# Performance work log

Hardware: AMD Instinct MI355X
Metric: run time of the kernel (lower is better)

The kernel has to match this reference:

```python
import jax, jax.numpy as jnp
import numpy as np

# ----- static layer configuration (mirrors __init__ / _precompute_cg_tensor) -----
NODE_LS = [0, 0, 1, 1]          # node_l_values (multiplicity expressed via repetition; node_multiplicity=1)
EDGE_SH = 1                      # edge_sh_degree
H_LS = NODE_LS + NODE_LS + [0]   # l-values of h = [f_src, f_tgt, d]
H_DIMS = [2 * l + 1 for l in H_LS]
H_OFF = np.concatenate([[0], np.cumsum(H_DIMS)])
A_DIMS = [2 * l + 1 for l in range(EDGE_SH + 1)]
A_OFF = np.concatenate([[0], np.cumsum(A_DIMS)])
O_DIMS = [2 * l + 1 for l in NODE_LS]
O_OFF = np.concatenate([[0], np.cumsum(O_DIMS)])
F_DIM = int(O_OFF[-1])           # 8
A_DIM = int(A_OFF[-1])           # 4
N_NODES, N_EDGES = 100000, 1600000
MLP_DIMS = [2 * len(NODE_LS) + 1, 64, 32, len(NODE_LS)]  # 9 -> 64 -> 32 -> 4

def _levi_civita():
    e = np.zeros((3, 3, 3), np.float32)
    e[0, 1, 2] = e[1, 2, 0] = e[2, 0, 1] = 1.0
    e[0, 2, 1] = e[2, 1, 0] = e[1, 0, 2] = -1.0
    return e

# real SO(3) Clebsch-Gordan tensors (e3nn wigner_3j normalization: full contraction norm 1)
_CG = {
    (0, 0, 0): np.ones((1, 1, 1), np.float32),
    (0, 1, 1): (np.eye(3, dtype=np.float32) / np.sqrt(3.0)).reshape(1, 3, 3),
    (1, 0, 1): (np.eye(3, dtype=np.float32) / np.sqrt(3.0)).reshape(3, 1, 3),
    (1, 1, 0): (np.eye(3, dtype=np.float32) / np.sqrt(3.0)).reshape(3, 3, 1),
    (1, 1, 1): _levi_civita() / np.sqrt(6.0),
}

CONNECTIONS = []  # (h_idx, a_l, out_idx, cg[h,a,o]) -- same enumeration order as the torch loop
for _h_idx, _hl in enumerate(H_LS):
    for _al in range(EDGE_SH + 1):
        for _oi, _ol in enumerate(NODE_LS):
            if abs(_hl - _al) <= _ol <= _hl + _al and (_hl, _al, _ol) in _CG:
                CONNECTIONS.append((_h_idx, _al, _oi, jnp.asarray(_CG[(_hl, _al, _ol)])))


def _invariants(x):
    # s_i = [f_{l=0}, ||f_{l=1}||, ...] per l-slot (multiplicity 1)
    outs = []
    for i, l in enumerate(NODE_LS):
        s, e = int(O_OFF[i]), int(O_OFF[i + 1])
        if l == 0:
            outs.append(x[:, s:e])
        else:
            outs.append(jnp.linalg.norm(x[:, s:e], axis=1, keepdims=True))
    return jnp.concatenate(outs, axis=1)


def setup_inputs() -> dict:
    ks = jax.random.split(jax.random.key(0), 10)
    edge_index = jax.random.randint(ks[0], (2, N_EDGES), 0, N_NODES)
    f = jax.random.normal(ks[1], (N_NODES, F_DIM), jnp.float32)
    d = jax.random.uniform(ks[2], (N_EDGES, 1), jnp.float32)
    a = jax.random.normal(ks[3], (N_EDGES, A_DIM), jnp.float32)
    w1 = jax.random.normal(ks[4], (EDGE_SH + 1,), jnp.float32) * 0.1
    w2 = jax.random.normal(ks[5], (EDGE_SH + 1,), jnp.float32) * 0.1
    W0 = jax.random.normal(ks[6], (MLP_DIMS[0], MLP_DIMS[1]), jnp.float32) / np.sqrt(MLP_DIMS[0])
    b0 = jnp.zeros((MLP_DIMS[1],), jnp.float32)
    W1 = jax.random.normal(ks[7], (MLP_DIMS[1], MLP_DIMS[2]), jnp.float32) / np.sqrt(MLP_DIMS[1])
    b1 = jnp.zeros((MLP_DIMS[2],), jnp.float32)
    W2 = jax.random.normal(ks[8], (MLP_DIMS[2], MLP_DIMS[3]), jnp.float32) / np.sqrt(MLP_DIMS[2])
    b2 = jnp.zeros((MLP_DIMS[3],), jnp.float32)
    return {"edge_index": edge_index, "f": f, "d": d, "a": a, "w1": w1, "w2": w2,
            "W0": W0, "b0": b0, "W1": W1, "b1": b1, "W2": W2, "b2": b2}


def reference(edge_index, f, d, a, w1, w2, W0, b0, W1, b1, W2, b2):
    src, tgt = edge_index[0], edge_index[1]
    n = f.shape[0]
    h = jnp.concatenate([f[src], f[tgt], d], axis=1)  # [E, 17]
    messages = jnp.zeros((h.shape[0], F_DIM), f.dtype)
    for h_idx, a_l, out_idx, cg in CONNECTIONS:
        hs, he = int(H_OFF[h_idx]), int(H_OFF[h_idx + 1])
        as_, ae = int(A_OFF[a_l]), int(A_OFF[a_l + 1])
        os_, oe = int(O_OFF[out_idx]), int(O_OFF[out_idx + 1])
        raw = jnp.einsum('hao,eh,ea->eo', cg, h[:, hs:he], a[:, as_:ae])  # [E, 2*out_l+1]
        msg = jnp.tanh(w2[a_l] * jnp.tanh(w1[a_l] * raw))
        messages = messages.at[:, os_:oe].add(msg)
    agg = jax.ops.segment_sum(messages, tgt, num_segments=n)          # [N, 8]
    dist_sum = jax.ops.segment_sum(d, tgt, num_segments=n)           # [N, 1]
    counts = jax.ops.segment_sum(jnp.ones((h.shape[0],), f.dtype), tgt, num_segments=n)
    avg_d = dist_sum / (counts[:, None] + 1e-8)
    psi_in = jnp.concatenate([_invariants(f), _invariants(agg), avg_d], axis=1)  # [N, 9]
    x = jax.nn.relu(psi_in @ W0 + b0)
    x = jax.nn.relu(x @ W1 + b1)
    gates = jax.nn.sigmoid(x @ W2 + b2)  # [N, 4]
    gate_full = jnp.concatenate(
        [jnp.repeat(gates[:, i:i + 1], O_DIMS[i], axis=1) for i in range(len(NODE_LS))], axis=1)
    return f + gate_full * agg
```

## Files before the change

### kernel.cpp

```cpp
#include <hip/hip_runtime.h>
#include <math.h>

#define IS3 0.57735026918962576f
#define IS6 0.40824829046386302f

#define SHIFT 11
#define BSZ   2048
#define CAP   36864u
#define SEG   10
#define MQ    4096.0f
#define IMQ   (1.0f/4096.0f)

__device__ __forceinline__ float fastrcp(float x) { return __builtin_amdgcn_rcpf(x); }

__device__ __forceinline__ float Tnl(float x, float tw1, float w2) {
    float e = __expf(tw1 * x);
    float u = 1.0f - 2.0f * fastrcp(e + 1.0f);
    float z = w2 * u;
    float z2 = z * z;
    float p = __builtin_fmaf(z2, 0.133333333f, -0.333333333f);
    return __builtin_fmaf(z * z2, p, z);
}

__device__ __forceinline__ int q16(float x) {
    int v = (int)rintf(x * MQ);
    v = v >  32767 ?  32767 : v;
    v = v < -32768 ? -32768 : v;
    return v;
}

__global__ __launch_bounds__(1024) void route_kernel(
    const int* __restrict__ ei, const float* __restrict__ f,
    const float* __restrict__ d, const float* __restrict__ a,
    const float* __restrict__ w1p, const float* __restrict__ w2p,
    unsigned* __restrict__ tails,
    unsigned* __restrict__ qmeta,
    uint2* __restrict__ qmsg,
    int E, int nbuk)
{
    __shared__ unsigned hcnt[64];
    __shared__ unsigned hoff[64];
    int tid = threadIdx.x;
    if (tid < 64) hcnt[tid] = 0;
    __syncthreads();

    int e = blockIdx.x * 1024 + tid;
    bool valid = (e < E);
    int t = 0;
    unsigned b = 0, lrank = 0;
    if (valid) {
        t = ei[E + e];
        b = ((unsigned)t) >> SHIFT;
        lrank = atomicAdd(&hcnt[b], 1u);
    }
    __syncthreads();

    unsigned basek = 0;
    if (tid < nbuk && hcnt[tid] != 0u)
        basek = atomicAdd(&tails[tid * 64], hcnt[tid]);

    unsigned dq = 0;
    uint2 pk = make_uint2(0u, 0u);
    if (valid) {
        int s = ei[e];
        float tw10 = 2.0f * w1p[0], tw11 = 2.0f * w1p[1];
        float w20 = w2p[0], w21 = w2p[1];

        const float4* f4 = (const float4*)f;
        float4 sA = f4[2*s], sB = f4[2*s+1];
        float4 tA = f4[2*t], tB = f4[2*t+1];
        float de = d[e];
        float4 av = ((const float4*)a)[e];
        float a0 = av.x, ax = av.y, ay = av.z, az = av.w;

        float sc[5] = { sA.x, sA.y, tA.x, tA.y, de };
        float vx[4] = { sA.z, sB.y, tA.z, tB.y };
        float vy[4] = { sA.w, sB.z, tA.w, tB.z };
        float vz[4] = { sB.x, sB.w, tB.x, tB.w };

        float mS = 0.f, mX = 0.f, mY = 0.f, mZ = 0.f;
        #pragma unroll
        for (int i = 0; i < 5; ++i) {
            mS += Tnl(sc[i] * a0, tw10, w20);
            mX += Tnl(sc[i] * ax * IS3, tw11, w21);
            mY += Tnl(sc[i] * ay * IS3, tw11, w21);
            mZ += Tnl(sc[i] * az * IS3, tw11, w21);
        }
        #pragma unroll
        for (int i = 0; i < 4; ++i) {
            float dva = vx[i]*ax + vy[i]*ay + vz[i]*az;
            mS += Tnl(dva * IS3, tw11, w21);
            mX += Tnl(vx[i] * a0 * IS3, tw10, w20);
            mY += Tnl(vy[i] * a0 * IS3, tw10, w20);
            mZ += Tnl(vz[i] * a0 * IS3, tw10, w20);
            float cx = vy[i]*az - vz[i]*ay;
            float cy = vz[i]*ax - vx[i]*az;
            float cz = vx[i]*ay - vy[i]*ax;
            mX += Tnl(cx * IS6, tw11, w21);
            mY += Tnl(cy * IS6, tw11, w21);
            mZ += Tnl(cz * IS6, tw11, w21);
        }

        unsigned dqi = (unsigned)(de * 255.0f + 0.5f);
        dq = dqi > 255u ? 255u : dqi;
        int qS = q16(mS), qX = q16(mX), qY = q16(mY), qZ = q16(mZ);
        pk.x = ((unsigned)(unsigned short)qS) | (((unsigned)(unsigned short)qX) << 16);
        pk.y = ((unsigned)(unsigned short)qY) | (((unsigned)(unsigned short)qZ) << 16);
    }

    if (tid < nbuk) hoff[tid] = basek;
    __syncthreads();

    if (valid) {
        unsigned pos = hoff[b] + lrank;
        if (pos < CAP) {
            size_t idx = (size_t)b * CAP + pos;
            qmeta[idx] = (((unsigned)(t & (BSZ - 1))) << 8) | dq;
            qmsg[idx]  = pk;
        }
    }
}

__global__ __launch_bounds__(1024) void bucket_kernel(
    const unsigned* __restrict__ tails, const unsigned* __restrict__ qmeta,
    const uint2* __restrict__ qmsg, unsigned* __restrict__ partial, int nbuk)
{
    __shared__ unsigned long long acc1[BSZ];
    __shared__ unsigned long long acc2[BSZ];
    int wg = blockIdx.x;
    int b = wg / SEG, sgi = wg % SEG;
    for (int i = threadIdx.x; i < BSZ; i += 1024) { acc1[i] = 0ull; acc2[i] = 0ull; }
    __syncthreads();

    unsigned tail = tails[b * 64];
    if (tail > CAP) tail = CAP;
    unsigned lo = (tail * (unsigned)sgi) / SEG;
    unsigned hi = (tail * (unsigned)(sgi + 1)) / SEG;
    size_t base = (size_t)b * CAP;

    for (unsigned q = lo + threadIdx.x; q < hi; q += 1024) {
        unsigned meta = qmeta[base + q];
        uint2 m = qmsg[base + q];
        int local = (int)(meta >> 8);
        unsigned dq8 = meta & 255u;
        unsigned Sb = (m.x & 0xFFFFu) ^ 0x8000u;
        unsigned Xb = (m.x >> 16)     ^ 0x8000u;
        unsigned Yb = (m.y & 0xFFFFu) ^ 0x8000u;
        unsigned Zb = (m.y >> 16)     ^ 0x8000u;
        unsigned long long v1 = (unsigned long long)Sb
            | ((unsigned long long)Xb << 24) | (1ull << 48);
        unsigned long long v2 = (unsigned long long)Yb
            | ((unsigned long long)Zb << 24) | ((unsigned long long)dq8 << 48);
        atomicAdd(&acc1[local], v1);
        atomicAdd(&acc2[local], v2);
    }
    __syncthreads();

    unsigned* dst = partial + (size_t)wg * (BSZ * 4);
    for (int i = threadIdx.x; i < BSZ; i += 1024) {
        unsigned long long u1 = acc1[i], u2 = acc2[i];
        dst[0*BSZ + i] = (unsigned)u1;
        dst[1*BSZ + i] = (unsigned)(u1 >> 32);
        dst[2*BSZ + i] = (unsigned)u2;
        dst[3*BSZ + i] = (unsigned)(u2 >> 32);
    }
}

__global__ __launch_bounds__(128) void mlp_kernel(
    const float* __restrict__ f, const unsigned* __restrict__ partial,
    const float* __restrict__ W0, const float* __restrict__ b0,
    const float* __restrict__ W1, const float* __restrict__ b1,
    const float* __restrict__ W2, const float* __restrict__ b2,
    float* __restrict__ out, int N)
{
    __shared__ float4 sW0t4[64*3];
    __shared__ float4 sW1v[64*8];
    __shared__ float4 sW2v[32];
    __shared__ float  sb0[64];
    __shared__ float4 sb1v[8];
    __shared__ float4 sb2v[1];

    int tid = threadIdx.x;
    float* w0t = (float*)sW0t4;
    for (int idx = tid; idx < 576; idx += 128) {
        int k = idx >> 6, i = idx & 63;
        w0t[i * 12 + k] = W0[idx];
    }
    for (int idx = tid; idx < 192; idx += 128) {
        int i = idx / 3, k = 9 + idx % 3;
        w0t[i * 12 + k] = 0.f;
    }
    { float* p = (float*)sW1v; for (int idx = tid; idx < 2048; idx += 128) p[idx] = W1[idx]; }
    { float* p = (float*)sW2v; if (tid < 128) p[tid] = W2[tid]; }
    if (tid < 64) sb0[tid] = b0[tid];
    { float* p = (float*)sb1v; if (tid < 32) p[tid] = b1[tid]; }
    { float* p = (float*)sb2v; if (tid < 4)  p[tid] = b2[tid]; }
    __syncthreads();

    int n = blockIdx.x * 128 + tid;
    if (n >= N) return;

    int b = n >> SHIFT;
    int local = n & (BSZ - 1);
    int S = 0, X = 0, Y = 0, Z = 0, cnt = 0, dqs = 0;
    #pragma unroll
    for (int s2 = 0; s2 < SEG; ++s2) {
        const unsigned* p = partial + ((size_t)(b * SEG + s2)) * (BSZ * 4);
        unsigned long long u1 = (unsigned long long)p[0*BSZ + local]
                              | ((unsigned long long)p[1*BSZ + local] << 32);
        unsigned long long u2 = (unsigned long long)p[2*BSZ + local]
                              | ((unsigned long long)p[3*BSZ + local] << 32);
        int c = (int)(u1 >> 48);
        S += (int)(u1 & 0xFFFFFF) - (c << 15);
        X += (int)((u1 >> 24) & 0xFFFFFF) - (c << 15);
        Y += (int)(u2 & 0xFFFFFF) - (c << 15);
        Z += (int)((u2 >> 24) & 0xFFFFFF) - (c << 15);
        dqs += (int)(u2 >> 48);
        cnt += c;
    }
    float aS = (float)S * IMQ, ax = (float)X * IMQ;
    float ay = (float)Y * IMQ, az = (float)Z * IMQ;
    float cf = (float)cnt;
    float dsum = (float)dqs * (1.0f / 255.0f);

    float4 fA = ((const float4*)f)[2*n];
    float4 fB = ((const float4*)f)[2*n+1];

    float nrm1 = sqrtf(fA.z*fA.z + fA.w*fA.w + fB.x*fB.x);
    float nrm2 = sqrtf(fB.y*fB.y + fB.z*fB.z + fB.w*fB.w);
    float nv   = sqrtf(ax*ax + ay*ay + az*az);
    float avgd = dsum * fastrcp(cf + 1e-8f);
    float4 p0 = make_float4(fA.x, fA.y, nrm1, nrm2);
    float4 p1 = make_float4(aS, aS, nv, nv);
    float4 p2 = make_float4(avgd, 0.f, 0.f, 0.f);

    float x1s[32];
    #pragma unroll
    for (int j = 0; j < 8; ++j) {
        float4 bv = sb1v[j];
        x1s[4*j+0] = bv.x; x1s[4*j+1] = bv.y; x1s[4*j+2] = bv.z; x1s[4*j+3] = bv.w;
    }
    #pragma unroll
    for (int i = 0; i < 64; ++i) {
        float4 r0 = sW0t4[i*3+0], r1 = sW0t4[i*3+1], r2 = sW0t4[i*3+2];
        float acc = sb0[i]
            + r0.x*p0.x + r0.y*p0.y + r0.z*p0.z + r0.w*p0.w
            + r1.x*p1.x + r1.y*p1.y + r1.z*p1.z + r1.w*p1.w
            + r2.x*p2.x;
        acc = fmaxf(acc, 0.f);
        #pragma unroll
        for (int j = 0; j < 8; ++j) {
            float4 wv = sW1v[i*8+j];
            x1s[4*j+0] += acc * wv.x;
            x1s[4*j+1] += acc * wv.y;
            x1s[4*j+2] += acc * wv.z;
            x1s[4*j+3] += acc * wv.w;
        }
    }
    #pragma unroll
    for (int j = 0; j < 32; ++j) x1s[j] = fmaxf(x1s[j], 0.f);

    float4 gb = sb2v[0];
    float g0 = gb.x, g1 = gb.y, g2 = gb.z, g3 = gb.w;
    #pragma unroll
    for (int i = 0; i < 32; ++i) {
        float4 wv = sW2v[i];
        g0 += x1s[i] * wv.x;
        g1 += x1s[i] * wv.y;
        g2 += x1s[i] * wv.z;
        g3 += x1s[i] * wv.w;
    }
    g0 = fastrcp(1.0f + __expf(-g0));
    g1 = fastrcp(1.0f + __expf(-g1));
    g2 = fastrcp(1.0f + __expf(-g2));
    g3 = fastrcp(1.0f + __expf(-g3));

    float* o = out + (size_t)8*n;
    o[0] = fA.x + g0*aS;
    o[1] = fA.y + g1*aS;
    o[2] = fA.z + g2*ax;
    o[3] = fA.w + g2*ay;
    o[4] = fB.x + g2*az;
    o[5] = fB.y + g3*ax;
    o[6] = fB.z + g3*ay;
    o[7] = fB.w + g3*az;
}

extern "C" void kernel_launch(void* const* d_in, const int* in_sizes, int n_in,
                              void* d_out, int out_size, void* d_ws, size_t ws_size,
                              hipStream_t stream) {
    const int*   ei = (const int*)d_in[0];
    const float* f  = (const float*)d_in[1];
    const float* d  = (const float*)d_in[2];
    const float* a  = (const float*)d_in[3];
    const float* w1 = (const float*)d_in[4];
    const float* w2 = (const float*)d_in[5];
    const float* W0 = (const float*)d_in[6];
    const float* b0 = (const float*)d_in[7];
    const float* W1 = (const float*)d_in[8];
    const float* b1 = (const float*)d_in[9];
    const float* W2 = (const float*)d_in[10];
    const float* b2 = (const float*)d_in[11];
    int E = in_sizes[0] / 2;
    int N = in_sizes[1] / 8;
    int nbuk = (N + BSZ - 1) >> SHIFT;

    char* w = (char*)d_ws;
    size_t qn = (size_t)nbuk * CAP;
    uint2*    qmsg    = (uint2*)w;
    unsigned* qmeta   = (unsigned*)(w + qn * 8);
    unsigned* partial = (unsigned*)(w + qn * 12);
    unsigned* tails   = (unsigned*)(w + qn * 12
                        + (size_t)nbuk * SEG * BSZ * 4 * 4);

    hipMemsetAsync(tails, 0, (size_t)nbuk * 64 * sizeof(unsigned), stream);

    int EB = (E + 1023) / 1024;
    route_kernel <<<dim3(EB), dim3(1024), 0, stream>>>(
        ei, f, d, a, w1, w2, tails, qmeta, qmsg, E, nbuk);
    bucket_kernel<<<dim3(nbuk * SEG), dim3(1024), 0, stream>>>(
        tails, qmeta, qmsg, partial, nbuk);
    mlp_kernel   <<<dim3((N + 127) / 128), dim3(128), 0, stream>>>(
        f, partial, W0, b0, W1, b1, W2, b2, (float*)d_out, N);
}
```

Measured before the change: 178.0 us.

## Fuse bucket accumulation with gating MLP, one workgroup per 256-node sub-bucket

Merges the bucket aggregation and MLP kernels into one launch. Each workgroup owns a 256-node slice of a bucket, scans the whole bucket queue, and keeps only entries whose meta field names its slice. It accumulates into a small shared array and runs the MLP directly on the result. This drops the global partial-sum buffer, its write and read traffic, and one kernel launch. In exchange each bucket's queue metadata is read eight times, and only 256 of 1024 threads do MLP work.

```diff
diff --git a/kernel.cpp b/kernel.cpp
--- a/kernel.cpp
+++ b/kernel.cpp
@@ -7,7 +7,8 @@
 #define SHIFT 11
 #define BSZ   2048
 #define CAP   36864u
-#define SEG   10
+#define SEG   8
+#define SUB   256
 #define MQ    4096.0f
 #define IMQ   (1.0f/4096.0f)
 
@@ -121,58 +122,16 @@
     }
 }
 
-__global__ __launch_bounds__(1024) void bucket_kernel(
+__global__ __launch_bounds__(1024) void bucket_mlp_kernel(
     const unsigned* __restrict__ tails, const unsigned* __restrict__ qmeta,
-    const uint2* __restrict__ qmsg, unsigned* __restrict__ partial, int nbuk)
-{
-    __shared__ unsigned long long acc1[BSZ];
-    __shared__ unsigned long long acc2[BSZ];
-    int wg = blockIdx.x;
-    int b = wg / SEG, sgi = wg % SEG;
-    for (int i = threadIdx.x; i < BSZ; i += 1024) { acc1[i] = 0ull; acc2[i] = 0ull; }
-    __syncthreads();
-
-    unsigned tail = tails[b * 64];
-    if (tail > CAP) tail = CAP;
-    unsigned lo = (tail * (unsigned)sgi) / SEG;
-    unsigned hi = (tail * (unsigned)(sgi + 1)) / SEG;
-    size_t base = (size_t)b * CAP;
-
-    for (unsigned q = lo + threadIdx.x; q < hi; q += 1024) {
-        unsigned meta = qmeta[base + q];
-        uint2 m = qmsg[base + q];
-        int local = (int)(meta >> 8);
-        unsigned dq8 = meta & 255u;
-        unsigned Sb = (m.x & 0xFFFFu) ^ 0x8000u;
-        unsigned Xb = (m.x >> 16)     ^ 0x8000u;
-        unsigned Yb = (m.y & 0xFFFFu) ^ 0x8000u;
-        unsigned Zb = (m.y >> 16)     ^ 0x8000u;
-        unsigned long long v1 = (unsigned long long)Sb
-            | ((unsigned long long)Xb << 24) | (1ull << 48);
-        unsigned long long v2 = (unsigned long long)Yb
-            | ((unsigned long long)Zb << 24) | ((unsigned long long)dq8 << 48);
-        atomicAdd(&acc1[local], v1);
-        atomicAdd(&acc2[local], v2);
-    }
-    __syncthreads();
-
-    unsigned* dst = partial + (size_t)wg * (BSZ * 4);
-    for (int i = threadIdx.x; i < BSZ; i += 1024) {
-        unsigned long long u1 = acc1[i], u2 = acc2[i];
-        dst[0*BSZ + i] = (unsigned)u1;
-        dst[1*BSZ + i] = (unsigned)(u1 >> 32);
-        dst[2*BSZ + i] = (unsigned)u2;
-        dst[3*BSZ + i] = (unsigned)(u2 >> 32);
-    }
-}
-
-__global__ __launch_bounds__(128) void mlp_kernel(
-    const float* __restrict__ f, const unsigned* __restrict__ partial,
+    const uint2* __restrict__ qmsg, const float* __restrict__ f,
     const float* __restrict__ W0, const float* __restrict__ b0,
     const float* __restrict__ W1, const float* __restrict__ b1,
     const float* __restrict__ W2, const float* __restrict__ b2,
     float* __restrict__ out, int N)
 {
+    __shared__ unsigned long long acc1[SUB];
+    __shared__ unsigned long long acc2[SUB];
     __shared__ float4 sW0t4[64*3];
     __shared__ float4 sW1v[64*8];
     __shared__ float4 sW2v[32];
@@ -181,43 +140,62 @@
     __shared__ float4 sb2v[1];
 
     int tid = threadIdx.x;
+    int wg = blockIdx.x;
+    int b = wg >> 3, sgi = wg & 7;
+
+    if (tid < SUB) { acc1[tid] = 0ull; acc2[tid] = 0ull; }
     float* w0t = (float*)sW0t4;
-    for (int idx = tid; idx < 576; idx += 128) {
-        int k = idx >> 6, i = idx & 63;
-        w0t[i * 12 + k] = W0[idx];
-    }
-    for (int idx = tid; idx < 192; idx += 128) {
-        int i = idx / 3, k = 9 + idx % 3;
+    if (tid < 576) {
+        int k = tid >> 6, i = tid & 63;
+        w0t[i * 12 + k] = W0[tid];
+    }
+    if (tid < 192) {
+        int i = tid / 3, k = 9 + tid % 3;
         w0t[i * 12 + k] = 0.f;
     }
-    { float* p = (float*)sW1v; for (int idx = tid; idx < 2048; idx += 128) p[idx] = W1[idx]; }
+    { float* p = (float*)sW1v; for (int idx = tid; idx < 2048; idx += 1024) p[idx] = W1[idx]; }
     { float* p = (float*)sW2v; if (tid < 128) p[tid] = W2[tid]; }
     if (tid < 64) sb0[tid] = b0[tid];
     { float* p = (float*)sb1v; if (tid < 32) p[tid] = b1[tid]; }
     { float* p = (float*)sb2v; if (tid < 4)  p[tid] = b2[tid]; }
     __syncthreads();
 
-    int n = blockIdx.x * 128 + tid;
+    unsigned tail = tails[b * 64];
+    if (tail > CAP) tail = CAP;
+    size_t base = (size_t)b * CAP;
+
+    for (unsigned q = tid; q < tail; q += 1024) {
+        unsigned meta = qmeta[base + q];
+        if ((meta >> 16) == (unsigned)sgi) {
+            uint2 m = qmsg[base + q];
+            int local = (int)((meta >> 8) & (SUB - 1));
+            unsigned dq8 = meta & 255u;
+            unsigned Sb = (m.x & 0xFFFFu) ^ 0x8000u;
+            unsigned Xb = (m.x >> 16)     ^ 0x8000u;
+            unsigned Yb = (m.y & 0xFFFFu) ^ 0x8000u;
+            unsigned Zb = (m.y >> 16)     ^ 0x8000u;
+            unsigned long long v1 = (unsigned long long)Sb
+                | ((unsigned long long)Xb << 24) | (1ull << 48);
+            unsigned long long v2 = (unsigned long long)Yb
+                | ((unsigned long long)Zb << 24) | ((unsigned long long)dq8 << 48);
+            atomicAdd(&acc1[local], v1);
+            atomicAdd(&acc2[local], v2);
+        }
+    }
+    __syncthreads();
+
+    if (tid >= SUB) return;
+    int n = b * BSZ + sgi * SUB + tid;
     if (n >= N) return;
 
-    int b = n >> SHIFT;
-    int local = n & (BSZ - 1);
-    int S = 0, X = 0, Y = 0, Z = 0, cnt = 0, dqs = 0;
-    #pragma unroll
-    for (int s2 = 0; s2 < SEG; ++s2) {
-        const unsigned* p = partial + ((size_t)(b * SEG + s2)) * (BSZ * 4);
-        unsigned long long u1 = (unsigned long long)p[0*BSZ + local]
-                              | ((unsigned long long)p[1*BSZ + local] << 32);
-        unsigned long long u2 = (unsigned long long)p[2*BSZ + local]
-                              | ((unsigned long long)p[3*BSZ + local] << 32);
-        int c = (int)(u1 >> 48);
-        S += (int)(u1 & 0xFFFFFF) - (c << 15);
-        X += (int)((u1 >> 24) & 0xFFFFFF) - (c << 15);
-        Y += (int)(u2 & 0xFFFFFF) - (c << 15);
-        Z += (int)((u2 >> 24) & 0xFFFFFF) - (c << 15);
-        dqs += (int)(u2 >> 48);
-        cnt += c;
-    }
+    unsigned long long u1 = acc1[tid], u2 = acc2[tid];
+    int cnt = (int)(u1 >> 48);
+    int S = (int)(u1 & 0xFFFFFF) - (cnt << 15);
+    int X = (int)((u1 >> 24) & 0xFFFFFF) - (cnt << 15);
+    int Y = (int)(u2 & 0xFFFFFF) - (cnt << 15);
+    int Z = (int)((u2 >> 24) & 0xFFFFFF) - (cnt << 15);
+    int dqs = (int)(u2 >> 48);
+
     float aS = (float)S * IMQ, ax = (float)X * IMQ;
     float ay = (float)Y * IMQ, az = (float)Z * IMQ;
     float cf = (float)cnt;
@@ -307,19 +285,15 @@
 
     char* w = (char*)d_ws;
     size_t qn = (size_t)nbuk * CAP;
-    uint2*    qmsg    = (uint2*)w;
-    unsigned* qmeta   = (unsigned*)(w + qn * 8);
-    unsigned* partial = (unsigned*)(w + qn * 12);
-    unsigned* tails   = (unsigned*)(w + qn * 12
-                        + (size_t)nbuk * SEG * BSZ * 4 * 4);
+    uint2*    qmsg  = (uint2*)w;
+    unsigned* qmeta = (unsigned*)(w + qn * 8);
+    unsigned* tails = (unsigned*)(w + qn * 12);
 
     hipMemsetAsync(tails, 0, (size_t)nbuk * 64 * sizeof(unsigned), stream);
 
     int EB = (E + 1023) / 1024;
-    route_kernel <<<dim3(EB), dim3(1024), 0, stream>>>(
+    route_kernel<<<dim3(EB), dim3(1024), 0, stream>>>(
         ei, f, d, a, w1, w2, tails, qmeta, qmsg, E, nbuk);
-    bucket_kernel<<<dim3(nbuk * SEG), dim3(1024), 0, stream>>>(
-        tails, qmeta, qmsg, partial, nbuk);
-    mlp_kernel   <<<dim3((N + 127) / 128), dim3(128), 0, stream>>>(
-        f, partial, W0, b0, W1, b1, W2, b2, (float*)d_out, N);
-}
+    bucket_mlp_kernel<<<dim3(nbuk * SEG), dim3(1024), 0, stream>>>(
+        tails, qmeta, qmsg, f, W0, b0, W1, b1, W2, b2, (float*)d_out, N);
+}
```

New measurement: 222.4 us. +24.9%, slower.
